# Optimization experiments

Measured on AMD Instinct MI355X. Metric: run time of the kernel, lower is better.

The kernel has to match this reference:

```python
import jax, jax.numpy as jnp
import numpy as np

# Each of the 16 soft logic gates op_i(a,b) is linear in the basis {1, a, b, a*b}.
# Row i gives (c_const, c_a, c_b, c_ab) for gate i (standard difflogic ordering,
# gate 3 = A pass-through, gate 1 = AND, gate 6 = XOR, etc.).
_M = jnp.array([
    [0, 0, 0, 0],   # 0: False
    [0, 0, 0, 1],   # 1: a AND b
    [0, 1, 0, -1],  # 2: a AND NOT b
    [0, 1, 0, 0],   # 3: a
    [0, 0, 1, -1],  # 4: NOT a AND b
    [0, 0, 1, 0],   # 5: b
    [0, 1, 1, -2],  # 6: a XOR b
    [0, 1, 1, -1],  # 7: a OR b
    [1, -1, -1, 1], # 8: NOT (a OR b)
    [1, -1, -1, 2], # 9: NOT (a XOR b)
    [1, 0, -1, 0],  # 10: NOT b
    [1, 0, -1, 1],  # 11: a OR NOT b
    [1, -1, 0, 0],  # 12: NOT a
    [1, -1, 0, 1],  # 13: NOT a OR b
    [1, 0, 0, -1],  # 14: NOT (a AND b)
    [1, 0, 0, 0],   # 15: True
], dtype=jnp.float32)

B, C, H, W = 16, 3, 64, 64
K, DEPTH, RF, STRIDE = 32, 4, 5, 1
S = 2 ** DEPTH            # 16 leaf pairs per tree
OUT_H = (H - RF) // STRIDE + 1  # 60
OUT_W = (W - RF) // STRIDE + 1  # 60
P = OUT_H * OUT_W         # 3600 sliding positions


def setup_inputs() -> dict:
    key = jax.random.key(0)
    ks = jax.random.split(key, 12)
    x = jax.random.uniform(ks[0], (B, C, H, W), dtype=jnp.float32)

    # Random (h, w, c) pairs inside the receptive field, per kernel / leaf slot
    # (connections='random'): relative offsets in [0, RF) x [0, RF) x [0, C).
    def rel(k1, k2, k3):
        rh = jax.random.randint(k1, (K, S), 0, RF)
        rw = jax.random.randint(k2, (K, S), 0, RF)
        rc = jax.random.randint(k3, (K, S), 0, C)
        return rh, rw, rc

    rha, rwa, rca = rel(ks[1], ks[2], ks[3])
    rhb, rwb, rcb = rel(ks[4], ks[5], ks[6])

    # Expand relative offsets over all sliding-window positions -> absolute indices.
    oh, ow = jnp.meshgrid(jnp.arange(OUT_H), jnp.arange(OUT_W), indexing='ij')
    oh = (oh.reshape(-1) * STRIDE)[None, :, None]  # (1, P, 1)
    ow = (ow.reshape(-1) * STRIDE)[None, :, None]

    def absolute(rh, rw, rc):
        ah = oh + rh[:, None, :]                       # (K, P, S)
        aw = ow + rw[:, None, :]
        ac = jnp.broadcast_to(rc[:, None, :], (K, P, S))
        return ah.astype(jnp.int32), aw.astype(jnp.int32), ac.astype(jnp.int32)

    ah, aw, ac = absolute(rha, rwa, rca)
    bh, bw, bc = absolute(rhb, rwb, rcb)

    # Gate-selection logits per tree level: level l has 2**(DEPTH-l) gates,
    # each with (K, 16) logits (weight_init='random').
    ws = {}
    for l in range(DEPTH + 1):
        n = 2 ** (DEPTH - l)
        ws[f'w{l}'] = jax.random.normal(ks[7 + l], (n, K, 16), dtype=jnp.float32)

    return dict(x=x, ah=ah, aw=aw, ac=ac, bh=bh, bw=bw, bc=bc, **ws)


def _bin_op(a, b, w):
    """Weighted mix of 16 soft logic gates.

    a, b: (B, K, P, S);  w: (S, K, 16) raw logits, soft_raw = softmax.
    """
    coef = jax.nn.softmax(w, axis=-1) @ _M           # (S, K, 4)
    coef = jnp.transpose(coef, (2, 1, 0))[:, :, None, :]  # (4, K, 1, S)
    return coef[0] + coef[1] * a + coef[2] * b + coef[3] * (a * b)


def reference(x, ah, aw, ac, bh, bw, bc, w0, w1, w2, w3, w4):
    # Level 0: irregular gather of feature pairs over (c, h, w).
    a = x[:, ac, ah, aw]   # (B, K, P, S)
    b = x[:, bc, bh, bw]
    cur = _bin_op(a, b, w0)
    # Higher levels: combine adjacent sibling nodes (even/odd) along node dim.
    for w in (w1, w2, w3, w4):
        cur = _bin_op(cur[..., 0::2], cur[..., 1::2], w)
    # cur: (B, K, P, 1) -> (B, K, OUT_H, OUT_W)
    return cur.reshape(cur.shape[0], cur.shape[1], OUT_H, OUT_W)
```

## Files before the change

### kernel.cpp

```cpp
#include <hip/hip_runtime.h>

#define B_   16
#define C_   3
#define H_   64
#define W_   64
#define K_   32
#define S_   16
#define OH_  60
#define OW_  60
#define P_   3600

#define KG   4
#define NKG  (K_/KG)
#define NBQ  4
#define ROWS (C_*5)
#define BP   4
#define ROWSTRIDE (W_*BP)
#define XLDS (ROWS*ROWSTRIDE)

__device__ __forceinline__ float gate(float4 c, float a, float b) {
    return fmaf(fmaf(c.w, a, c.z), b, fmaf(c.y, a, c.x));
}

__global__ __launch_bounds__(256, 4) void logic_fused_kernel(
    const float* __restrict__ x,
    const int* __restrict__ ah, const int* __restrict__ aw, const int* __restrict__ ac,
    const int* __restrict__ bh_, const int* __restrict__ bw_, const int* __restrict__ bc_,
    const float* __restrict__ w0, const float* __restrict__ w1,
    const float* __restrict__ w2, const float* __restrict__ w3,
    const float* __restrict__ w4,
    float* __restrict__ out)
{
    __shared__ float  xs[XLDS];
    __shared__ float4 cf[KG * 31];
    __shared__ int    bAi[KG * S_], bBi[KG * S_];

    const int oh  = blockIdx.x;
    const int bq  = blockIdx.y;
    const int kg  = blockIdx.z;
    const int tid = threadIdx.x;
    const int l   = tid & 63;
    const int wv  = tid >> 6;

    {
        const int b  = l & 3;
        const int w0 = l >> 2;
        const int gb = bq * 4 + b;
        for (int job = wv; job < ROWS * 4; job += 4) {
            int wb  = job & 3;
            int row = job >> 2;
            int c   = row >= 10 ? 2 : (row >= 5 ? 1 : 0);
            int dh  = row - 5 * c;
            int w   = w0 + 16 * wb;
            xs[row * ROWSTRIDE + w * BP + b] =
                x[((gb * C_ + c) * H_ + (oh + dh)) * W_ + w];
        }
    }

    if (tid < 128) {
        int node = tid & 31, kk = tid >> 5;
        if (node < 31) {
            int k = kg * KG + kk;
            const float* w; int i;
            if      (node < 16) { w = w0; i = node;      }
            else if (node < 24) { w = w1; i = node - 16; }
            else if (node < 28) { w = w2; i = node - 24; }
            else if (node < 30) { w = w3; i = node - 28; }
            else                { w = w4; i = 0;         }
            const float* src = w + ((size_t)i * K_ + k) * 16;
            float lg[16];
            float m = -1e30f;
#pragma unroll
            for (int s = 0; s < 16; ++s) { lg[s] = src[s]; m = fmaxf(m, lg[s]); }
            float sum = 0.f;
#pragma unroll
            for (int s = 0; s < 16; ++s) { lg[s] = expf(lg[s] - m); sum += lg[s]; }
            float inv = 1.f / sum;
            const float M[16][4] = {
                {0,0,0,0},{0,0,0,1},{0,1,0,-1},{0,1,0,0},
                {0,0,1,-1},{0,0,1,0},{0,1,1,-2},{0,1,1,-1},
                {1,-1,-1,1},{1,-1,-1,2},{1,0,-1,0},{1,0,-1,1},
                {1,-1,0,0},{1,-1,0,1},{1,0,0,-1},{1,0,0,0}};
            float c0 = 0.f, c1 = 0.f, c2 = 0.f, c3 = 0.f;
#pragma unroll
            for (int s = 0; s < 16; ++s) {
                float pr = lg[s] * inv;
                c0 += pr * M[s][0]; c1 += pr * M[s][1];
                c2 += pr * M[s][2]; c3 += pr * M[s][3];
            }
            cf[kk * 31 + node] = make_float4(c0, c1, c2, c3);
        }
    } else {
        int i = tid - 128;
        int s = i & 15;
        if (i < 64) {
            int kk = i >> 4;
            int k  = kg * KG + kk;
            int idx = k * (P_ * 16) + s;
            bAi[kk * 16 + s] = (ac[idx] * 5 + ah[idx]) * ROWSTRIDE + aw[idx] * BP;
        } else {
            int kk = (i - 64) >> 4;
            int k  = kg * KG + kk;
            int idx = k * (P_ * 16) + s;
            bBi[kk * 16 + s] = (bc_[idx] * 5 + bh_[idx]) * ROWSTRIDE + bw_[idx] * BP;
        }
    }
    __syncthreads();

    const int k      = kg * KG + wv;
    const int ow     = l;
    const int ow_eff = ow < OW_ ? ow : OW_ - 1;
    const int lo     = ow_eff * BP;

    int baseA[S_], baseB[S_];
#pragma unroll
    for (int s = 0; s < S_; ++s) {
        baseA[s] = __builtin_amdgcn_readfirstlane(bAi[wv * 16 + s]);
        baseB[s] = __builtin_amdgcn_readfirstlane(bBi[wv * 16 + s]);
    }

    const float4* cfw = &cf[wv * 31];

    float t[4][8];
#pragma unroll
    for (int i = 0; i < 8; ++i) {
        float4 a0 = *(const float4*)&xs[baseA[2*i]   + lo];
        float4 b0 = *(const float4*)&xs[baseB[2*i]   + lo];
        float4 a1 = *(const float4*)&xs[baseA[2*i+1] + lo];
        float4 b1 = *(const float4*)&xs[baseB[2*i+1] + lo];
        float4 c0 = cfw[2*i], c1 = cfw[2*i+1];
        float4 d  = cfw[16 + i];
        {
            float la = gate(c0, a0.x, b0.x), lb = gate(c1, a1.x, b1.x);
            t[0][i] = gate(d, la, lb);
        }
        {
            float la = gate(c0, a0.y, b0.y), lb = gate(c1, a1.y, b1.y);
            t[1][i] = gate(d, la, lb);
        }
        {
            float la = gate(c0, a0.z, b0.z), lb = gate(c1, a1.z, b1.z);
            t[2][i] = gate(d, la, lb);
        }
        {
            float la = gate(c0, a0.w, b0.w), lb = gate(c1, a1.w, b1.w);
            t[3][i] = gate(d, la, lb);
        }
    }
#pragma unroll
    for (int i = 0; i < 4; ++i) {
        float4 c = cfw[24 + i];
#pragma unroll
        for (int j = 0; j < 4; ++j)
            t[j][i] = gate(c, t[j][2*i], t[j][2*i+1]);
    }
#pragma unroll
    for (int i = 0; i < 2; ++i) {
        float4 c = cfw[28 + i];
#pragma unroll
        for (int j = 0; j < 4; ++j)
            t[j][i] = gate(c, t[j][2*i], t[j][2*i+1]);
    }
    {
        float4 c = cfw[30];
        if (ow < OW_) {
            const int obase = k * P_ + oh * OW_ + ow;
#pragma unroll
            for (int j = 0; j < 4; ++j) {
                float r = gate(c, t[j][0], t[j][1]);
                out[(size_t)(bq * 4 + j) * (K_ * P_) + obase] = r;
            }
        }
    }
}

extern "C" void kernel_launch(void* const* d_in, const int* in_sizes, int n_in,
                              void* d_out, int out_size, void* d_ws, size_t ws_size,
                              hipStream_t stream) {
    const float* x  = (const float*)d_in[0];
    const int* ah = (const int*)d_in[1];
    const int* aw = (const int*)d_in[2];
    const int* ac = (const int*)d_in[3];
    const int* bh = (const int*)d_in[4];
    const int* bw = (const int*)d_in[5];
    const int* bc = (const int*)d_in[6];
    const float* w0 = (const float*)d_in[7];
    const float* w1 = (const float*)d_in[8];
    const float* w2 = (const float*)d_in[9];
    const float* w3 = (const float*)d_in[10];
    const float* w4 = (const float*)d_in[11];
    float* out = (float*)d_out;

    dim3 grid(OH_, NBQ, NKG);
    logic_fused_kernel<<<grid, 256, 0, stream>>>(x, ah, aw, ac, bh, bw, bc,
                                                 w0, w1, w2, w3, w4, out);
}
```

Baseline: 30.19 us.

## Split coefficient/index prep into separate kernel and use packed v2f FMA gates

Moves the per-block softmax coefficient computation and gather-index setup into a small prep kernel that writes to workspace, so each main block only copies precomputed values into LDS. Rewrites the gate arithmetic to use two-wide float vectors so the compiler can emit packed FP32 FMA instructions, processing two batch lanes per op. The cost is an extra kernel launch and a dependency between the two kernels, in exchange for removing redundant expf/softmax work repeated across all 1920 blocks and halving the FMA instruction count.

After: 68.31 us. +126.3%, slower.

```diff
diff --git a/kernel.cpp b/kernel.cpp
--- a/kernel.cpp
+++ b/kernel.cpp
@@ -1,4 +1,6 @@
 #include <hip/hip_runtime.h>
+
+typedef float v2f __attribute__((ext_vector_type(2)));
 
 #define B_   16
 #define C_   3
@@ -18,17 +20,74 @@
 #define ROWSTRIDE (W_*BP)
 #define XLDS (ROWS*ROWSTRIDE)
 
-__device__ __forceinline__ float gate(float4 c, float a, float b) {
-    return fmaf(fmaf(c.w, a, c.z), b, fmaf(c.y, a, c.x));
-}
-
-__global__ __launch_bounds__(256, 4) void logic_fused_kernel(
-    const float* __restrict__ x,
+__device__ __forceinline__ v2f gate2(float4 c, v2f a, v2f b) {
+    v2f cx = {c.x, c.x}, cy = {c.y, c.y}, cz = {c.z, c.z}, cw = {c.w, c.w};
+    return __builtin_elementwise_fma(__builtin_elementwise_fma(cw, a, cz), b,
+                                     __builtin_elementwise_fma(cy, a, cx));
+}
+
+__global__ __launch_bounds__(256) void prep_kernel(
     const int* __restrict__ ah, const int* __restrict__ aw, const int* __restrict__ ac,
-    const int* __restrict__ bh_, const int* __restrict__ bw_, const int* __restrict__ bc_,
+    const int* __restrict__ bh, const int* __restrict__ bw, const int* __restrict__ bc,
     const float* __restrict__ w0, const float* __restrict__ w1,
     const float* __restrict__ w2, const float* __restrict__ w3,
     const float* __restrict__ w4,
+    float4* __restrict__ cfg, int* __restrict__ bAg, int* __restrict__ bBg)
+{
+    const int blk = blockIdx.x, tid = threadIdx.x;
+    if (blk < 4) {
+        int t = blk * 256 + tid;
+        if (t >= 31 * K_) return;
+        int node = t >> 5, k = t & 31;
+        const float* w; int i;
+        if      (node < 16) { w = w0; i = node;      }
+        else if (node < 24) { w = w1; i = node - 16; }
+        else if (node < 28) { w = w2; i = node - 24; }
+        else if (node < 30) { w = w3; i = node - 28; }
+        else                { w = w4; i = 0;         }
+        const float* src = w + ((size_t)i * K_ + k) * 16;
+        float lg[16];
+        float m = -1e30f;
+#pragma unroll
+        for (int s = 0; s < 16; ++s) { lg[s] = src[s]; m = fmaxf(m, lg[s]); }
+        float sum = 0.f;
+#pragma unroll
+        for (int s = 0; s < 16; ++s) { lg[s] = expf(lg[s] - m); sum += lg[s]; }
+        float inv = 1.f / sum;
+        const float M[16][4] = {
+            {0,0,0,0},{0,0,0,1},{0,1,0,-1},{0,1,0,0},
+            {0,0,1,-1},{0,0,1,0},{0,1,1,-2},{0,1,1,-1},
+            {1,-1,-1,1},{1,-1,-1,2},{1,0,-1,0},{1,0,-1,1},
+            {1,-1,0,0},{1,-1,0,1},{1,0,0,-1},{1,0,0,0}};
+        float c0 = 0.f, c1 = 0.f, c2 = 0.f, c3 = 0.f;
+#pragma unroll
+        for (int s = 0; s < 16; ++s) {
+            float pr = lg[s] * inv;
+            c0 += pr * M[s][0]; c1 += pr * M[s][1];
+            c2 += pr * M[s][2]; c3 += pr * M[s][3];
+        }
+        cfg[k * 31 + node] = make_float4(c0, c1, c2, c3);
+    } else {
+#pragma unroll
+        for (int rep = 0; rep < 4; ++rep) {
+            int idx = rep * 256 + tid;
+            if (idx < 512) {
+                int k = idx >> 4, s = idx & 15;
+                int j = k * (P_ * 16) + s;
+                bAg[idx] = (ac[j] * 5 + ah[j]) * ROWSTRIDE + aw[j] * BP;
+            } else {
+                int i2 = idx - 512;
+                int k = i2 >> 4, s = i2 & 15;
+                int j = k * (P_ * 16) + s;
+                bBg[i2] = (bc[j] * 5 + bh[j]) * ROWSTRIDE + bw[j] * BP;
+            }
+        }
+    }
+}
+
+__global__ __launch_bounds__(256, 4) void logic_main_kernel(
+    const float* __restrict__ x, const float4* __restrict__ cfg,
+    const int* __restrict__ bAg, const int* __restrict__ bBg,
     float* __restrict__ out)
 {
     __shared__ float  xs[XLDS];
@@ -56,53 +115,19 @@
                 x[((gb * C_ + c) * H_ + (oh + dh)) * W_ + w];
         }
     }
-
     if (tid < 128) {
-        int node = tid & 31, kk = tid >> 5;
-        if (node < 31) {
-            int k = kg * KG + kk;
-            const float* w; int i;
-            if      (node < 16) { w = w0; i = node;      }
-            else if (node < 24) { w = w1; i = node - 16; }
-            else if (node < 28) { w = w2; i = node - 24; }
-            else if (node < 30) { w = w3; i = node - 28; }
-            else                { w = w4; i = 0;         }
-            const float* src = w + ((size_t)i * K_ + k) * 16;
-            float lg[16];
-            float m = -1e30f;
-#pragma unroll
-            for (int s = 0; s < 16; ++s) { lg[s] = src[s]; m = fmaxf(m, lg[s]); }
-            float sum = 0.f;
-#pragma unroll
-            for (int s = 0; s < 16; ++s) { lg[s] = expf(lg[s] - m); sum += lg[s]; }
-            float inv = 1.f / sum;
-            const float M[16][4] = {
-                {0,0,0,0},{0,0,0,1},{0,1,0,-1},{0,1,0,0},
-                {0,0,1,-1},{0,0,1,0},{0,1,1,-2},{0,1,1,-1},
-                {1,-1,-1,1},{1,-1,-1,2},{1,0,-1,0},{1,0,-1,1},
-                {1,-1,0,0},{1,-1,0,1},{1,0,0,-1},{1,0,0,0}};
-            float c0 = 0.f, c1 = 0.f, c2 = 0.f, c3 = 0.f;
-#pragma unroll
-            for (int s = 0; s < 16; ++s) {
-                float pr = lg[s] * inv;
-                c0 += pr * M[s][0]; c1 += pr * M[s][1];
-                c2 += pr * M[s][2]; c3 += pr * M[s][3];
-            }
-            cf[kk * 31 + node] = make_float4(c0, c1, c2, c3);
-        }
+        int kk = tid >> 5, node = tid & 31;
+        if (node < 31)
+            cf[kk * 31 + node] = cfg[(kg * KG + kk) * 31 + node];
     } else {
         int i = tid - 128;
-        int s = i & 15;
         if (i < 64) {
-            int kk = i >> 4;
-            int k  = kg * KG + kk;
-            int idx = k * (P_ * 16) + s;
-            bAi[kk * 16 + s] = (ac[idx] * 5 + ah[idx]) * ROWSTRIDE + aw[idx] * BP;
+            int k = kg * KG + (i >> 4);
+            bAi[i] = bAg[k * 16 + (i & 15)];
         } else {
-            int kk = (i - 64) >> 4;
-            int k  = kg * KG + kk;
-            int idx = k * (P_ * 16) + s;
-            bBi[kk * 16 + s] = (bc_[idx] * 5 + bh_[idx]) * ROWSTRIDE + bw_[idx] * BP;
+            int i2 = i - 64;
+            int k = kg * KG + (i2 >> 4);
+            bBi[i2] = bBg[k * 16 + (i2 & 15)];
         }
     }
     __syncthreads();
@@ -121,55 +146,52 @@
 
     const float4* cfw = &cf[wv * 31];
 
-    float t[4][8];
-#pragma unroll
-    for (int i = 0; i < 8; ++i) {
-        float4 a0 = *(const float4*)&xs[baseA[2*i]   + lo];
-        float4 b0 = *(const float4*)&xs[baseB[2*i]   + lo];
-        float4 a1 = *(const float4*)&xs[baseA[2*i+1] + lo];
-        float4 b1 = *(const float4*)&xs[baseB[2*i+1] + lo];
-        float4 c0 = cfw[2*i], c1 = cfw[2*i+1];
-        float4 d  = cfw[16 + i];
-        {
-            float la = gate(c0, a0.x, b0.x), lb = gate(c1, a1.x, b1.x);
-            t[0][i] = gate(d, la, lb);
-        }
-        {
-            float la = gate(c0, a0.y, b0.y), lb = gate(c1, a1.y, b1.y);
-            t[1][i] = gate(d, la, lb);
-        }
-        {
-            float la = gate(c0, a0.z, b0.z), lb = gate(c1, a1.z, b1.z);
-            t[2][i] = gate(d, la, lb);
-        }
-        {
-            float la = gate(c0, a0.w, b0.w), lb = gate(c1, a1.w, b1.w);
-            t[3][i] = gate(d, la, lb);
+    v2f t0[8], t1[8];
+#pragma unroll
+    for (int g = 0; g < 4; ++g) {
+        float4 A[4], Bv[4];
+#pragma unroll
+        for (int m = 0; m < 4; ++m) {
+            A[m]  = *(const float4*)&xs[baseA[4*g + m] + lo];
+            Bv[m] = *(const float4*)&xs[baseB[4*g + m] + lo];
+        }
+#pragma unroll
+        for (int m = 0; m < 2; ++m) {
+            const int s0 = 2 * m;
+            const int n1 = 2 * g + m;
+            float4 c0 = cfw[4*g + s0], c1 = cfw[4*g + s0 + 1], d = cfw[16 + n1];
+            v2f a0l = {A[s0].x,  A[s0].y},   a0h = {A[s0].z,  A[s0].w};
+            v2f b0l = {Bv[s0].x, Bv[s0].y},  b0h = {Bv[s0].z, Bv[s0].w};
+            v2f a1l = {A[s0+1].x, A[s0+1].y}, a1h = {A[s0+1].z, A[s0+1].w};
+            v2f b1l = {Bv[s0+1].x,Bv[s0+1].y},b1h = {Bv[s0+1].z,Bv[s0+1].w};
+            v2f l0l = gate2(c0, a0l, b0l), l0h = gate2(c0, a0h, b0h);
+            v2f l1l = gate2(c1, a1l, b1l), l1h = gate2(c1, a1h, b1h);
+            t0[n1] = gate2(d, l0l, l1l);
+            t1[n1] = gate2(d, l0h, l1h);
         }
     }
 #pragma unroll
     for (int i = 0; i < 4; ++i) {
         float4 c = cfw[24 + i];
-#pragma unroll
-        for (int j = 0; j < 4; ++j)
-            t[j][i] = gate(c, t[j][2*i], t[j][2*i+1]);
+        t0[i] = gate2(c, t0[2*i], t0[2*i+1]);
+        t1[i] = gate2(c, t1[2*i], t1[2*i+1]);
     }
 #pragma unroll
     for (int i = 0; i < 2; ++i) {
         float4 c = cfw[28 + i];
-#pragma unroll
-        for (int j = 0; j < 4; ++j)
-            t[j][i] = gate(c, t[j][2*i], t[j][2*i+1]);
+        t0[i] = gate2(c, t0[2*i], t0[2*i+1]);
+        t1[i] = gate2(c, t1[2*i], t1[2*i+1]);
     }
     {
         float4 c = cfw[30];
+        v2f r0 = gate2(c, t0[0], t0[1]);
+        v2f r1 = gate2(c, t1[0], t1[1]);
         if (ow < OW_) {
-            const int obase = k * P_ + oh * OW_ + ow;
-#pragma unroll
-            for (int j = 0; j < 4; ++j) {
-                float r = gate(c, t[j][0], t[j][1]);
-                out[(size_t)(bq * 4 + j) * (K_ * P_) + obase] = r;
-            }
+            const size_t obase = (size_t)k * P_ + oh * OW_ + ow;
+            out[(size_t)(bq*4 + 0) * (K_*P_) + obase] = r0.x;
+            out[(size_t)(bq*4 + 1) * (K_*P_) + obase] = r0.y;
+            out[(size_t)(bq*4 + 2) * (K_*P_) + obase] = r1.x;
+            out[(size_t)(bq*4 + 3) * (K_*P_) + obase] = r1.y;
         }
     }
 }
@@ -191,7 +213,13 @@
     const float* w4 = (const float*)d_in[11];
     float* out = (float*)d_out;
 
+    float4* cfg = (float4*)d_ws;
+    int*    bAg = (int*)(cfg + 31 * K_);
+    int*    bBg = bAg + K_ * S_;
+
+    prep_kernel<<<5, 256, 0, stream>>>(ah, aw, ac, bh, bw, bc,
+                                       w0, w1, w2, w3, w4, cfg, bAg, bBg);
+
     dim3 grid(OH_, NBQ, NKG);
-    logic_fused_kernel<<<grid, 256, 0, stream>>>(x, ah, aw, ac, bh, bw, bc,
-                                                 w0, w1, w2, w3, w4, out);
-}
+    logic_main_kernel<<<grid, 256, 0, stream>>>(x, cfg, bAg, bBg, out);
+}
```
